# Kernel tuning notes

Measured on AMD Instinct MI355X. Metric: run time of the kernel, lower is better.

The kernel has to match this reference:

```python
import jax, jax.numpy as jnp
import numpy as np


def setup_inputs() -> dict:
    key = jax.random.key(0)
    k1, k2 = jax.random.split(key)
    B, S, V = 8, 512, 30522
    logits = jax.random.normal(k1, (B, S, V), dtype=jnp.float32)
    attention_mask = jax.random.randint(k2, (B, S), 0, 2, dtype=jnp.int32)
    return {"logits": logits, "attention_mask": attention_mask, "top_k": 64}


def reference(logits, attention_mask, top_k):
    # Fused SPLADE activation: log1p(relu(logits)) * mask, max-pooled over seq.
    mask = attention_mask.astype(logits.dtype)[:, :, None]        # (B, S, 1)
    activated = jnp.log1p(jax.nn.relu(logits)) * mask             # (B, S, V)
    values = jnp.max(activated, axis=1)                           # (B, V)
    # Top-k thresholding: zero out everything below the k-th largest value.
    top_values, _ = jax.lax.top_k(values, top_k)                  # (B, k)
    threshold = top_values[..., -1, None]                         # (B, 1)
    return values * (values >= threshold).astype(values.dtype)
```

## Files before the change

### kernel.cpp

```cpp
#include <hip/hip_runtime.h>
#include <hip/hip_bf16.h>

constexpr int B_ = 8;
constexpr int S_ = 512;
constexpr int V_ = 30522;

constexpr int K1_BLOCK = 256;
constexpr int K1_VEC   = 2;
constexpr int K1_COLS  = K1_BLOCK * K1_VEC;
constexpr int NVCHUNK  = (V_ + K1_COLS - 1) / K1_COLS;
constexpr int NSCHUNK  = 2;
constexpr int SCHUNK   = S_ / NSCHUNK;

__global__ __launch_bounds__(K1_BLOCK)
void splade_max_kernel(const float* __restrict__ logits,
                       const int* __restrict__ mask,
                       unsigned int* __restrict__ out_bits)
{
    __shared__ int s_idx[SCHUNK];
    __shared__ int s_cnt;
    const int b  = blockIdx.z;
    const int s0 = blockIdx.y * SCHUNK;

    if (threadIdx.x == 0) s_cnt = 0;
    __syncthreads();
    for (int i = threadIdx.x; i < SCHUNK; i += K1_BLOCK) {
        if (mask[b * S_ + s0 + i] != 0) {
            const int p = atomicAdd(&s_cnt, 1);
            s_idx[p] = i;
        }
    }
    __syncthreads();
    const int n = s_cnt;

    const int c0 = (blockIdx.x * K1_BLOCK + threadIdx.x) * K1_VEC;
    if (c0 >= V_) return;

    const float* base = logits + (size_t)(b * S_ + s0) * V_ + c0;
    float m0 = 0.0f, m1 = 0.0f;
    for (int j = 0; j < n; ++j) {
        const int s = s_idx[j];
        const float2 x = *reinterpret_cast<const float2*>(base + (size_t)s * V_);
        m0 = fmaxf(m0, x.x);
        m1 = fmaxf(m1, x.y);
    }
    unsigned int* o = out_bits + (size_t)b * V_ + c0;
    atomicMax(o,     __float_as_uint(m0));
    atomicMax(o + 1, __float_as_uint(m1));
}

constexpr int K2_BLOCK = 1024;
constexpr int NPT = (V_ + K2_BLOCK - 1) / K2_BLOCK;

__global__ __launch_bounds__(K2_BLOCK)
void splade_topk_kernel(unsigned int* __restrict__ vals_bits,
                        const int* __restrict__ topk_ptr)
{
    const int b = blockIdx.x;
    const int k = topk_ptr[0];
    unsigned int* row = vals_bits + (size_t)b * V_;

    unsigned int v[NPT];
#pragma unroll
    for (int i = 0; i < NPT; ++i) {
        const int idx = threadIdx.x + i * K2_BLOCK;
        v[i] = (idx < V_) ? row[idx] : 0u;
    }

    __shared__ int s_cnt;
    unsigned int lo = 0u, hi = 0x7f800000u;
    while (hi - lo > 1u) {
        const unsigned int mid = lo + ((hi - lo) >> 1);
        int c = 0;
#pragma unroll
        for (int i = 0; i < NPT; ++i) {
            const int idx = threadIdx.x + i * K2_BLOCK;
            c += (idx < V_ && v[i] >= mid) ? 1 : 0;
        }
        for (int off = 32; off > 0; off >>= 1)
            c += __shfl_down(c, off);
        if (threadIdx.x == 0) s_cnt = 0;
        __syncthreads();
        if ((threadIdx.x & 63) == 0) atomicAdd(&s_cnt, c);
        __syncthreads();
        const int cnt = s_cnt;
        if (cnt >= k) lo = mid; else hi = mid;
        __syncthreads();
    }

    const unsigned int T = lo;
    float* frow = reinterpret_cast<float*>(row);
#pragma unroll
    for (int i = 0; i < NPT; ++i) {
        const int idx = threadIdx.x + i * K2_BLOCK;
        if (idx < V_) {
            const float m = __uint_as_float(v[i]);
            frow[idx] = (v[i] >= T) ? log1pf(m) : 0.0f;
        }
    }
}

extern "C" void kernel_launch(void* const* d_in, const int* in_sizes, int n_in,
                              void* d_out, int out_size, void* d_ws, size_t ws_size,
                              hipStream_t stream) {
    const float* logits = (const float*)d_in[0];
    const int*   mask   = (const int*)d_in[1];
    const int*   topk   = (const int*)d_in[2];

    hipMemsetAsync(d_out, 0, (size_t)out_size * sizeof(float), stream);

    dim3 g1(NVCHUNK, NSCHUNK, B_);
    splade_max_kernel<<<g1, K1_BLOCK, 0, stream>>>(logits, mask, (unsigned int*)d_out);
    splade_topk_kernel<<<B_, K2_BLOCK, 0, stream>>>((unsigned int*)d_out, topk);
}
```

Measured before the change: 89.88 us.

## Drop sequence split and memset, unroll gathered-row max loop by eight

New measurement: 84.00 us. -6.5%, faster.

```diff
diff --git a/kernel.cpp b/kernel.cpp
--- a/kernel.cpp
+++ b/kernel.cpp
@@ -9,62 +9,71 @@
 constexpr int K1_VEC   = 2;
 constexpr int K1_COLS  = K1_BLOCK * K1_VEC;
 constexpr int NVCHUNK  = (V_ + K1_COLS - 1) / K1_COLS;
-constexpr int NSCHUNK  = 2;
-constexpr int SCHUNK   = S_ / NSCHUNK;
 
 __global__ __launch_bounds__(K1_BLOCK)
 void splade_max_kernel(const float* __restrict__ logits,
                        const int* __restrict__ mask,
-                       unsigned int* __restrict__ out_bits)
+                       float* __restrict__ out)
 {
-    __shared__ int s_idx[SCHUNK];
+    __shared__ int s_idx[S_];
     __shared__ int s_cnt;
-    const int b  = blockIdx.z;
-    const int s0 = blockIdx.y * SCHUNK;
+    const int b = blockIdx.y;
 
     if (threadIdx.x == 0) s_cnt = 0;
     __syncthreads();
-    for (int i = threadIdx.x; i < SCHUNK; i += K1_BLOCK) {
-        if (mask[b * S_ + s0 + i] != 0) {
-            const int p = atomicAdd(&s_cnt, 1);
-            s_idx[p] = i;
-        }
-    }
+    for (int i = threadIdx.x; i < S_; i += K1_BLOCK)
+        if (mask[b * S_ + i] != 0)
+            s_idx[atomicAdd(&s_cnt, 1)] = i;
     __syncthreads();
     const int n = s_cnt;
 
     const int c0 = (blockIdx.x * K1_BLOCK + threadIdx.x) * K1_VEC;
     if (c0 >= V_) return;
 
-    const float* base = logits + (size_t)(b * S_ + s0) * V_ + c0;
+    const float* base = logits + (size_t)b * S_ * V_ + c0;
     float m0 = 0.0f, m1 = 0.0f;
-    for (int j = 0; j < n; ++j) {
-        const int s = s_idx[j];
-        const float2 x = *reinterpret_cast<const float2*>(base + (size_t)s * V_);
+
+    int j = 0;
+    for (; j + 8 <= n; j += 8) {
+        const int i0 = s_idx[j+0], i1 = s_idx[j+1], i2 = s_idx[j+2], i3 = s_idx[j+3];
+        const int i4 = s_idx[j+4], i5 = s_idx[j+5], i6 = s_idx[j+6], i7 = s_idx[j+7];
+        const float2 x0 = *reinterpret_cast<const float2*>(base + (size_t)i0 * V_);
+        const float2 x1 = *reinterpret_cast<const float2*>(base + (size_t)i1 * V_);
+        const float2 x2 = *reinterpret_cast<const float2*>(base + (size_t)i2 * V_);
+        const float2 x3 = *reinterpret_cast<const float2*>(base + (size_t)i3 * V_);
+        const float2 x4 = *reinterpret_cast<const float2*>(base + (size_t)i4 * V_);
+        const float2 x5 = *reinterpret_cast<const float2*>(base + (size_t)i5 * V_);
+        const float2 x6 = *reinterpret_cast<const float2*>(base + (size_t)i6 * V_);
+        const float2 x7 = *reinterpret_cast<const float2*>(base + (size_t)i7 * V_);
+        m0 = fmaxf(m0, fmaxf(fmaxf(fmaxf(x0.x, x1.x), fmaxf(x2.x, x3.x)),
+                             fmaxf(fmaxf(x4.x, x5.x), fmaxf(x6.x, x7.x))));
+        m1 = fmaxf(m1, fmaxf(fmaxf(fmaxf(x0.y, x1.y), fmaxf(x2.y, x3.y)),
+                             fmaxf(fmaxf(x4.y, x5.y), fmaxf(x6.y, x7.y))));
+    }
+    for (; j < n; ++j) {
+        const float2 x = *reinterpret_cast<const float2*>(base + (size_t)s_idx[j] * V_);
         m0 = fmaxf(m0, x.x);
         m1 = fmaxf(m1, x.y);
     }
-    unsigned int* o = out_bits + (size_t)b * V_ + c0;
-    atomicMax(o,     __float_as_uint(m0));
-    atomicMax(o + 1, __float_as_uint(m1));
+    *reinterpret_cast<float2*>(out + (size_t)b * V_ + c0) = make_float2(m0, m1);
 }
 
 constexpr int K2_BLOCK = 1024;
 constexpr int NPT = (V_ + K2_BLOCK - 1) / K2_BLOCK;
 
 __global__ __launch_bounds__(K2_BLOCK)
-void splade_topk_kernel(unsigned int* __restrict__ vals_bits,
+void splade_topk_kernel(float* __restrict__ vals,
                         const int* __restrict__ topk_ptr)
 {
     const int b = blockIdx.x;
     const int k = topk_ptr[0];
-    unsigned int* row = vals_bits + (size_t)b * V_;
+    float* row = vals + (size_t)b * V_;
 
     unsigned int v[NPT];
 #pragma unroll
     for (int i = 0; i < NPT; ++i) {
         const int idx = threadIdx.x + i * K2_BLOCK;
-        v[i] = (idx < V_) ? row[idx] : 0u;
+        v[i] = (idx < V_) ? __float_as_uint(row[idx]) : 0u;
     }
 
     __shared__ int s_cnt;
@@ -73,10 +82,8 @@
         const unsigned int mid = lo + ((hi - lo) >> 1);
         int c = 0;
 #pragma unroll
-        for (int i = 0; i < NPT; ++i) {
-            const int idx = threadIdx.x + i * K2_BLOCK;
-            c += (idx < V_ && v[i] >= mid) ? 1 : 0;
-        }
+        for (int i = 0; i < NPT; ++i)
+            c += (v[i] >= mid) ? 1 : 0;
         for (int off = 32; off > 0; off >>= 1)
             c += __shfl_down(c, off);
         if (threadIdx.x == 0) s_cnt = 0;
@@ -89,13 +96,12 @@
     }
 
     const unsigned int T = lo;
-    float* frow = reinterpret_cast<float*>(row);
 #pragma unroll
     for (int i = 0; i < NPT; ++i) {
         const int idx = threadIdx.x + i * K2_BLOCK;
         if (idx < V_) {
             const float m = __uint_as_float(v[i]);
-            frow[idx] = (v[i] >= T) ? log1pf(m) : 0.0f;
+            row[idx] = (v[i] >= T) ? log1pf(m) : 0.0f;
         }
     }
 }
@@ -106,10 +112,9 @@
     const float* logits = (const float*)d_in[0];
     const int*   mask   = (const int*)d_in[1];
     const int*   topk   = (const int*)d_in[2];
+    float*       out    = (float*)d_out;
 
-    hipMemsetAsync(d_out, 0, (size_t)out_size * sizeof(float), stream);
-
-    dim3 g1(NVCHUNK, NSCHUNK, B_);
-    splade_max_kernel<<<g1, K1_BLOCK, 0, stream>>>(logits, mask, (unsigned int*)d_out);
-    splade_topk_kernel<<<B_, K2_BLOCK, 0, stream>>>((unsigned int*)d_out, topk);
+    dim3 g1(NVCHUNK, B_);
+    splade_max_kernel<<<g1, K1_BLOCK, 0, stream>>>(logits, mask, out);
+    splade_topk_kernel<<<B_, K2_BLOCK, 0, stream>>>(out, topk);
 }
```
